# Performance work log

Measured on AMD Instinct MI355X. Metric: run time of the kernel, lower is better.

## Reference

```python
import jax, jax.numpy as jnp
import numpy as np
from jax import lax

HEADS = 4
SR = 4
LN_EPS = 1e-5


def setup_inputs() -> dict:
    key = jax.random.key(0)
    ks = jax.random.split(key, 8)
    B, N, C = 8, 4096, 256
    w_scale = 0.05  # keep attention logits in a sane range
    return {
        "x": jax.random.normal(ks[0], (B, N, C), jnp.float32),
        "h": 64,
        "w": 64,
        "Wq": jax.random.normal(ks[1], (C, C), jnp.float32) * w_scale,
        "Wkv": jax.random.normal(ks[2], (C, 2 * C), jnp.float32) * w_scale,
        "sr_w": jax.random.normal(ks[3], (C, C, SR, SR), jnp.float32) * w_scale,
        "sr_b": jnp.zeros((C,), jnp.float32),
        "ln_g": jnp.ones((C,), jnp.float32),
        "ln_b": jnp.zeros((C,), jnp.float32),
        "Wo": jax.random.normal(ks[4], (C, C), jnp.float32) * w_scale,
        "bo": jnp.zeros((C,), jnp.float32),
    }


def _layernorm(x, g, b):
    mu = x.mean(-1, keepdims=True)
    var = ((x - mu) ** 2).mean(-1, keepdims=True)
    return (x - mu) * lax.rsqrt(var + LN_EPS) * g + b


def reference(x, h, w, Wq, Wkv, sr_w, sr_b, ln_g, ln_b, Wo, bo):
    B, N, C = x.shape
    hd = C // HEADS
    scale = hd ** -0.5
    # Q projection -> [B, H, N, hd]
    q = (x @ Wq).reshape(B, N, HEADS, hd).transpose(0, 2, 1, 3)
    # spatial reduction of K/V tokens: strided conv + LayerNorm
    x_kv = x.transpose(0, 2, 1).reshape(B, C, h, w)  # b (h w) c -> b c h w
    x_kv = lax.conv_general_dilated(
        x_kv, sr_w, window_strides=(SR, SR), padding="VALID",
        dimension_numbers=("NCHW", "OIHW", "NCHW"))
    x_kv = x_kv + sr_b[None, :, None, None]
    Nk = (h // SR) * (w // SR)
    x_kv = x_kv.reshape(B, C, Nk).transpose(0, 2, 1)  # b c h w -> b (h w) c
    x_kv = _layernorm(x_kv, ln_g, ln_b)
    # KV projection -> k, v each [B, H, Nk, hd]
    kv = (x_kv @ Wkv).reshape(B, Nk, 2, HEADS, hd)
    k = kv[:, :, 0].transpose(0, 2, 1, 3)
    v = kv[:, :, 1].transpose(0, 2, 1, 3)
    # attention: full [B, H, N, Nk] score matrix, softmax over kv axis
    att = jax.nn.softmax(jnp.einsum("bhxd,bhyd->bhxy", q, k) * scale, axis=-1)
    out = jnp.einsum("bhxy,bhyd->bhxd", att, v)
    out = out.transpose(0, 2, 1, 3).reshape(B, N, C)  # b h l d -> b l (h d)
    return out @ Wo + bo
```

## Files before the change

kernel.cpp:

```cpp
#include <hip/hip_runtime.h>

typedef __bf16 bf16;
typedef bf16 bf16x8 __attribute__((ext_vector_type(8)));
typedef bf16 bf16x4 __attribute__((ext_vector_type(4)));
typedef float f32x4 __attribute__((ext_vector_type(4)));

#define MFMA16(a, b, c) __builtin_amdgcn_mfma_f32_16x16x32_bf16(a, b, c, 0, 0, 0)
#define WAIT_LDS() __builtin_amdgcn_s_waitcnt(0xC07F)

__global__ void k_prep(const float* __restrict__ x, const float* __restrict__ Wq,
                       const float* __restrict__ Wkv, const float* __restrict__ Wo,
                       const float* __restrict__ srw,
                       bf16* __restrict__ x_bf, bf16* __restrict__ WqT,
                       bf16* __restrict__ WkvT, bf16* __restrict__ WoT,
                       bf16* __restrict__ srwT) {
  int bid = blockIdx.x, tid = threadIdx.x;
  if (bid < 8192) {
    int i = (bid * 256 + tid) * 4;
    float4 v = *(const float4*)(x + i);
    bf16x4 o;
    o[0] = (bf16)v.x; o[1] = (bf16)v.y; o[2] = (bf16)v.z; o[3] = (bf16)v.w;
    *(bf16x4*)(x_bf + i) = o;
  } else if (bid < 9216) {
    int id = (bid - 8192) * 256 + tid;
    if (id < 65536) {
      int c = id >> 8, r = id & 255;
      WqT[id] = (bf16)Wq[r * 256 + c];
    } else if (id < 196608) {
      int l = id - 65536;
      int c = l >> 8, r = l & 255;
      WkvT[l] = (bf16)Wkv[r * 512 + c];
    } else {
      int l = id - 196608;
      int c = l >> 8, r = l & 255;
      WoT[l] = (bf16)Wo[r * 256 + c];
    }
  } else {
    int id4 = ((bid - 9216) * 256 + tid) * 4;
    int o = id4 >> 12, rem = id4 & 4095;
    int i = rem >> 4, p = rem & 15;
    float4 v = *(const float4*)(srw + id4);
    srwT[(o << 12) + ((p + 0) << 8) + i] = (bf16)v.x;
    srwT[(o << 12) + ((p + 1) << 8) + i] = (bf16)v.y;
    srwT[(o << 12) + ((p + 2) << 8) + i] = (bf16)v.z;
    srwT[(o << 12) + ((p + 3) << 8) + i] = (bf16)v.w;
  }
}

template <int AMODE, int EMODE>
__global__ __launch_bounds__(256, 2) void k_gemm(
    const bf16* __restrict__ A, const bf16* __restrict__ Bt,
    void* __restrict__ Cout, const float* __restrict__ bias,
    int M, int N, int K) {
  constexpr int LDT = 72;
  __shared__ alignas(16) bf16 As[64 * LDT];
  __shared__ alignas(16) bf16 Bs[64 * LDT];
  int tid = threadIdx.x;
  int m0 = blockIdx.x * 64, n0 = blockIdx.y * 64;
  int kbeg = blockIdx.z * K;
  int wave = tid >> 6, lane = tid & 63;
  int quad = lane >> 4, l16 = lane & 15;

  f32x4 acc[4];
#pragma unroll
  for (int i = 0; i < 4; i++) acc[i] = (f32x4){0.f, 0.f, 0.f, 0.f};

  for (int k0 = kbeg; k0 < kbeg + K; k0 += 64) {
#pragma unroll
    for (int t = 0; t < 2; t++) {
      int c = tid + t * 256;
      int row = c >> 3, c8 = (c & 7) * 8;
      const bf16* asrc;
      if constexpr (AMODE == 0) {
        asrc = A + (size_t)(m0 + row) * K + k0 + c8;
      } else {
        int m = m0 + row;
        int b = m >> 8, tt = m & 255;
        int oh = tt >> 4, ow = tt & 15;
        int p = k0 >> 8;
        int kh = p >> 2, kw = p & 3;
        int tok = (oh * 4 + kh) * 64 + ow * 4 + kw;
        asrc = A + ((size_t)(b * 4096 + tok) << 8) + (k0 & 255) + c8;
      }
      *(bf16x8*)&As[row * LDT + c8] = *(const bf16x8*)asrc;
      *(bf16x8*)&Bs[row * LDT + c8] =
          *(const bf16x8*)(Bt + (size_t)(n0 + row) * ((AMODE == 1) ? 4096 : K) + k0 + c8);
    }
    __syncthreads();
#pragma unroll
    for (int kk = 0; kk < 64; kk += 32) {
      bf16x8 af = *(const bf16x8*)&As[(wave * 16 + l16) * LDT + kk + quad * 8];
#pragma unroll
      for (int nt = 0; nt < 4; nt++) {
        bf16x8 bfr = *(const bf16x8*)&Bs[(nt * 16 + l16) * LDT + kk + quad * 8];
        acc[nt] = MFMA16(af, bfr, acc[nt]);
      }
    }
    __syncthreads();
  }

  int rbase = m0 + wave * 16 + quad * 4;
#pragma unroll
  for (int nt = 0; nt < 4; nt++) {
    int col = n0 + nt * 16 + l16;
#pragma unroll
    for (int r = 0; r < 4; r++) {
      float v = acc[nt][r];
      int row = rbase + r;
      if constexpr (EMODE == 2) {
        int b = row >> 8, key = row & 255;
        int isv = col >> 8, c2 = col & 255;
        int hh = c2 >> 6, d = c2 & 63;
        int bh = b * 4 + hh;
        bf16* dst = (bf16*)Cout;
        if (isv == 0)
          dst[(((size_t)bh) * 256 + key) * 64 + d] = (bf16)v;
        else
          dst[32 * 256 * 64 + (((size_t)bh) * 64 + d) * 256 + key] = (bf16)v;
      } else if constexpr (EMODE == 3) {
        ((float*)Cout)[(size_t)row * N + col] = v + bias[col];
      } else {
        ((float*)Cout)[((size_t)blockIdx.z * M + row) * N + col] = v;
      }
    }
  }
}

__global__ void k_ln(const float* __restrict__ part, const float* __restrict__ srb,
                     const float* __restrict__ g, const float* __restrict__ bb,
                     bf16* __restrict__ out) {
  int row = blockIdx.x * 4 + (threadIdx.x >> 6);
  int lane = threadIdx.x & 63;
  size_t off = (size_t)row * 256 + lane * 4;
  float4 v = *(const float4*)&part[off];
#pragma unroll
  for (int z = 1; z < 8; z++) {
    float4 p = *(const float4*)&part[(size_t)z * 2048 * 256 + off];
    v.x += p.x; v.y += p.y; v.z += p.z; v.w += p.w;
  }
  int c = lane * 4;
  v.x += srb[c + 0]; v.y += srb[c + 1]; v.z += srb[c + 2]; v.w += srb[c + 3];
  float s = v.x + v.y + v.z + v.w;
#pragma unroll
  for (int i = 1; i < 64; i <<= 1) s += __shfl_xor(s, i, 64);
  float mu = s * (1.f / 256.f);
  float d0 = v.x - mu, d1 = v.y - mu, d2 = v.z - mu, d3 = v.w - mu;
  float q = d0 * d0 + d1 * d1 + d2 * d2 + d3 * d3;
#pragma unroll
  for (int i = 1; i < 64; i <<= 1) q += __shfl_xor(q, i, 64);
  float rs = rsqrtf(q * (1.f / 256.f) + 1e-5f);
  bf16x4 o;
  o[0] = (bf16)(d0 * rs * g[c + 0] + bb[c + 0]);
  o[1] = (bf16)(d1 * rs * g[c + 1] + bb[c + 1]);
  o[2] = (bf16)(d2 * rs * g[c + 2] + bb[c + 2]);
  o[3] = (bf16)(d3 * rs * g[c + 3] + bb[c + 3]);
  *(bf16x4*)&out[(size_t)row * 256 + c] = o;
}

__global__ __launch_bounds__(256, 2) void k_attn(
    const bf16* __restrict__ xbf,
    const bf16* __restrict__ WqT,
    const bf16* __restrict__ Kb,
    const bf16* __restrict__ Vt_g,
    bf16* __restrict__ O) {
  int qt = blockIdx.x, bh = blockIdx.y;
  int b = bh >> 2, h = bh & 3;
  int tid = threadIdx.x, wave = tid >> 6, lane = tid & 63;
  int quad = lane >> 4, l16 = lane & 15;

  __shared__ alignas(16) bf16 Ks[256 * 72];
  __shared__ alignas(16) bf16 Vt[64 * 264];
  __shared__ alignas(16) bf16 Qs[64 * 72];

  const bf16* Kbh = Kb + (size_t)bh * 256 * 64;
  const bf16* Vbh = Vt_g + (size_t)bh * 64 * 256;

#pragma unroll
  for (int t = 0; t < 8; t++) {
    int c = tid + t * 256;
    *(bf16x8*)&Ks[(c >> 3) * 72 + (c & 7) * 8] = *(const bf16x8*)&Kbh[c * 8];
    *(bf16x8*)&Vt[(c >> 5) * 264 + (c & 31) * 8] = *(const bf16x8*)&Vbh[c * 8];
  }

  const bf16* xrow  = xbf + ((size_t)(b * 4096 + qt * 64 + wave * 16 + l16) << 8) + quad * 8;
  const bf16* wqrow = WqT + ((size_t)(h * 64) << 8);
  f32x4 q[4];
#pragma unroll
  for (int i = 0; i < 4; i++) q[i] = (f32x4){0.f, 0.f, 0.f, 0.f};
#pragma unroll
  for (int k0 = 0; k0 < 256; k0 += 32) {
    bf16x8 ax = *(const bf16x8*)(xrow + k0);
#pragma unroll
    for (int nt = 0; nt < 4; nt++) {
      bf16x8 bw = *(const bf16x8*)&wqrow[((size_t)(nt * 16 + l16) << 8) + k0 + quad * 8];
      q[nt] = MFMA16(ax, bw, q[nt]);
    }
  }

#pragma unroll
  for (int nt = 0; nt < 4; nt++)
#pragma unroll
    for (int r = 0; r < 4; r++)
      Qs[(wave * 16 + quad * 4 + r) * 72 + nt * 16 + l16] = (bf16)q[nt][r];
  WAIT_LDS();
  bf16x8 aq0 = *(const bf16x8*)&Qs[(wave * 16 + l16) * 72 + 0 + quad * 8];
  bf16x8 aq1 = *(const bf16x8*)&Qs[(wave * 16 + l16) * 72 + 32 + quad * 8];
  __syncthreads();

  f32x4 s[16];
#pragma unroll
  for (int i = 0; i < 16; i++) s[i] = (f32x4){0.f, 0.f, 0.f, 0.f};
#pragma unroll
  for (int nt = 0; nt < 16; nt++) {
    bf16x8 b0 = *(const bf16x8*)&Ks[(nt * 16 + l16) * 72 + 0 + quad * 8];
    bf16x8 b1 = *(const bf16x8*)&Ks[(nt * 16 + l16) * 72 + 32 + quad * 8];
    s[nt] = MFMA16(aq0, b0, s[nt]);
    s[nt] = MFMA16(aq1, b1, s[nt]);
  }

  const float scale = 0.125f;
#pragma unroll
  for (int r = 0; r < 4; r++) {
    float m = -1e30f;
#pragma unroll
    for (int nt = 0; nt < 16; nt++) m = fmaxf(m, s[nt][r]);
#pragma unroll
    for (int i = 1; i < 16; i <<= 1) m = fmaxf(m, __shfl_xor(m, i, 64));
    float sum = 0.f;
#pragma unroll
    for (int nt = 0; nt < 16; nt++) {
      float e = __expf((s[nt][r] - m) * scale);
      s[nt][r] = e;
      sum += e;
    }
#pragma unroll
    for (int i = 1; i < 16; i <<= 1) sum += __shfl_xor(sum, i, 64);
    float inv = 1.f / sum;
#pragma unroll
    for (int nt = 0; nt < 16; nt++) s[nt][r] *= inv;
  }
  __syncthreads();

  bf16* Ps = Ks;
#pragma unroll
  for (int nt = 0; nt < 16; nt++)
#pragma unroll
    for (int r = 0; r < 4; r++)
      Ps[(wave * 16 + quad * 4 + r) * 264 + nt * 16 + l16] = (bf16)s[nt][r];
  WAIT_LDS();

  f32x4 o[4];
#pragma unroll
  for (int i = 0; i < 4; i++) o[i] = (f32x4){0.f, 0.f, 0.f, 0.f};
#pragma unroll
  for (int k0 = 0; k0 < 256; k0 += 32) {
    bf16x8 ap = *(const bf16x8*)&Ps[(wave * 16 + l16) * 264 + k0 + quad * 8];
#pragma unroll
    for (int nt = 0; nt < 4; nt++) {
      bf16x8 bv = *(const bf16x8*)&Vt[(nt * 16 + l16) * 264 + k0 + quad * 8];
      o[nt] = MFMA16(ap, bv, o[nt]);
    }
  }

  size_t orow = (size_t)b * 4096 + qt * 64 + wave * 16 + quad * 4;
#pragma unroll
  for (int nt = 0; nt < 4; nt++) {
    int col = h * 64 + nt * 16 + l16;
#pragma unroll
    for (int r = 0; r < 4; r++) O[(orow + r) * 256 + col] = (bf16)o[nt][r];
  }
}

extern "C" void kernel_launch(void* const* d_in, const int* in_sizes, int n_in,
                              void* d_out, int out_size, void* d_ws, size_t ws_size,
                              hipStream_t stream) {
  (void)in_sizes; (void)n_in; (void)out_size; (void)ws_size;
  const float* x   = (const float*)d_in[0];
  const float* Wq  = (const float*)d_in[3];
  const float* Wkv = (const float*)d_in[4];
  const float* srw = (const float*)d_in[5];
  const float* srb = (const float*)d_in[6];
  const float* lng = (const float*)d_in[7];
  const float* lnb = (const float*)d_in[8];
  const float* Wo  = (const float*)d_in[9];
  const float* bo  = (const float*)d_in[10];
  float* out = (float*)d_out;

  char* ws = (char*)d_ws;
  bf16*  x_bf  = (bf16*)(ws + 0);
  bf16*  AObuf = (bf16*)(ws + 16777216);
  float* convp = (float*)(ws + 33554432);
  bf16*  WqT   = (bf16*)(ws + 50331648);
  bf16*  WkvT  = (bf16*)(ws + 50462720);
  bf16*  WoT   = (bf16*)(ws + 50724864);
  bf16*  srwT  = (bf16*)(ws + 50855936);
  bf16*  xln   = (bf16*)(ws + 52953088);
  bf16*  kvbuf = (bf16*)(ws + 54001664);

  k_prep<<<10240, 256, 0, stream>>>(x, Wq, Wkv, Wo, srw, x_bf, WqT, WkvT, WoT, srwT);
  k_gemm<1, 4><<<dim3(32, 4, 8), 256, 0, stream>>>(x_bf, srwT, convp, nullptr, 2048, 256, 512);
  k_ln<<<512, 256, 0, stream>>>(convp, srb, lng, lnb, xln);
  k_gemm<0, 2><<<dim3(32, 8), 256, 0, stream>>>(xln, WkvT, kvbuf, nullptr, 2048, 512, 256);
  k_attn<<<dim3(64, 32), 256, 0, stream>>>(x_bf, WqT, kvbuf, kvbuf + (size_t)32 * 256 * 64, AObuf);
  k_gemm<0, 3><<<dim3(512, 4), 256, 0, stream>>>(AObuf, WoT, out, bo, 32768, 256, 256);
}
```

Baseline: 196.1 us.

## Make attention blocks persistent over four query tiles with register-resident Wq and prefetch

Each attention block now handles four consecutive 64-row query tiles, so K/V are loaded into LDS once per four tiles instead of once per tile. The Wq slice is kept in registers, and the next tile's x rows are loaded and projected to Q while the current tile's softmax and PV run, overlapping load latency with compute. Launch bounds drop to one block per SM-equivalent and the grid shrinks fourfold. The cost is much higher register use (32 bf16x8 for Wq plus prefetch buffers) and fewer blocks, which lowers occupancy and could leave CUs idle.

```diff
diff --git a/kernel.cpp b/kernel.cpp
--- a/kernel.cpp
+++ b/kernel.cpp
@@ -157,23 +157,25 @@
   *(bf16x4*)&out[(size_t)row * 256 + c] = o;
 }
 
-__global__ __launch_bounds__(256, 2) void k_attn(
+__global__ __launch_bounds__(256, 1) void k_attn(
     const bf16* __restrict__ xbf,
     const bf16* __restrict__ WqT,
     const bf16* __restrict__ Kb,
     const bf16* __restrict__ Vt_g,
     bf16* __restrict__ O) {
-  int qt = blockIdx.x, bh = blockIdx.y;
+  constexpr int ITERS = 4;
+  int qg = blockIdx.x, bh = blockIdx.y;
   int b = bh >> 2, h = bh & 3;
   int tid = threadIdx.x, wave = tid >> 6, lane = tid & 63;
   int quad = lane >> 4, l16 = lane & 15;
 
   __shared__ alignas(16) bf16 Ks[256 * 72];
   __shared__ alignas(16) bf16 Vt[64 * 264];
-  __shared__ alignas(16) bf16 Qs[64 * 72];
-
-  const bf16* Kbh = Kb + (size_t)bh * 256 * 64;
-  const bf16* Vbh = Vt_g + (size_t)bh * 64 * 256;
+  __shared__ alignas(16) bf16 Ps[64 * 264];
+
+  const bf16* Kbh   = Kb + (size_t)bh * 256 * 64;
+  const bf16* Vbh   = Vt_g + (size_t)bh * 64 * 256;
+  const bf16* wqrow = WqT + ((size_t)(h * 64) << 8);
 
 #pragma unroll
   for (int t = 0; t < 8; t++) {
@@ -182,92 +184,131 @@
     *(bf16x8*)&Vt[(c >> 5) * 264 + (c & 31) * 8] = *(const bf16x8*)&Vbh[c * 8];
   }
 
-  const bf16* xrow  = xbf + ((size_t)(b * 4096 + qt * 64 + wave * 16 + l16) << 8) + quad * 8;
-  const bf16* wqrow = WqT + ((size_t)(h * 64) << 8);
+  bf16x8 wqf[32];
+#pragma unroll
+  for (int k8 = 0; k8 < 8; k8++)
+#pragma unroll
+    for (int nt = 0; nt < 4; nt++)
+      wqf[k8 * 4 + nt] =
+          *(const bf16x8*)&wqrow[((size_t)(nt * 16 + l16) << 8) + k8 * 32 + quad * 8];
+
+  int qrow0 = b * 4096 + qg * (ITERS * 64) + wave * 16 + l16;
+  int pstripe = (wave * 16 + quad * 4) * 264;
+
   f32x4 q[4];
 #pragma unroll
   for (int i = 0; i < 4; i++) q[i] = (f32x4){0.f, 0.f, 0.f, 0.f};
-#pragma unroll
-  for (int k0 = 0; k0 < 256; k0 += 32) {
-    bf16x8 ax = *(const bf16x8*)(xrow + k0);
+  {
+    const bf16* xr = xbf + ((size_t)qrow0 << 8) + quad * 8;
+#pragma unroll
+    for (int k8 = 0; k8 < 8; k8++) {
+      bf16x8 ax = *(const bf16x8*)(xr + k8 * 32);
+#pragma unroll
+      for (int nt = 0; nt < 4; nt++) q[nt] = MFMA16(ax, wqf[k8 * 4 + nt], q[nt]);
+    }
+  }
+#pragma unroll
+  for (int nt = 0; nt < 4; nt++)
+#pragma unroll
+    for (int r = 0; r < 4; r++)
+      Ps[pstripe + r * 264 + nt * 16 + l16] = (bf16)q[nt][r];
+  WAIT_LDS();
+  bf16x8 aq0 = *(const bf16x8*)&Ps[(wave * 16 + l16) * 264 + 0 + quad * 8];
+  bf16x8 aq1 = *(const bf16x8*)&Ps[(wave * 16 + l16) * 264 + 32 + quad * 8];
+  __syncthreads();
+
+  for (int it = 0; it < ITERS; ++it) {
+    bool more = (it + 1 < ITERS);
+
+    f32x4 s[16];
+#pragma unroll
+    for (int i = 0; i < 16; i++) s[i] = (f32x4){0.f, 0.f, 0.f, 0.f};
+#pragma unroll
+    for (int nt = 0; nt < 16; nt++) {
+      bf16x8 b0 = *(const bf16x8*)&Ks[(nt * 16 + l16) * 72 + 0 + quad * 8];
+      bf16x8 b1 = *(const bf16x8*)&Ks[(nt * 16 + l16) * 72 + 32 + quad * 8];
+      s[nt] = MFMA16(aq0, b0, s[nt]);
+      s[nt] = MFMA16(aq1, b1, s[nt]);
+    }
+
+    bf16x8 xn[8];
+    if (more) {
+      const bf16* xr = xbf + ((size_t)(qrow0 + (it + 1) * 64) << 8) + quad * 8;
+#pragma unroll
+      for (int k8 = 0; k8 < 8; k8++) xn[k8] = *(const bf16x8*)(xr + k8 * 32);
+    }
+
+    const float scale = 0.125f;
+#pragma unroll
+    for (int r = 0; r < 4; r++) {
+      float m = -1e30f;
+#pragma unroll
+      for (int nt = 0; nt < 16; nt++) m = fmaxf(m, s[nt][r]);
+#pragma unroll
+      for (int i = 1; i < 16; i <<= 1) m = fmaxf(m, __shfl_xor(m, i, 64));
+      float sum = 0.f;
+#pragma unroll
+      for (int nt = 0; nt < 16; nt++) {
+        float e = __expf((s[nt][r] - m) * scale);
+        s[nt][r] = e;
+        sum += e;
+      }
+#pragma unroll
+      for (int i = 1; i < 16; i <<= 1) sum += __shfl_xor(sum, i, 64);
+      float inv = 1.f / sum;
+#pragma unroll
+      for (int nt = 0; nt < 16; nt++) s[nt][r] *= inv;
+    }
+
+    f32x4 qn[4];
+#pragma unroll
+    for (int i = 0; i < 4; i++) qn[i] = (f32x4){0.f, 0.f, 0.f, 0.f};
+    if (more) {
+#pragma unroll
+      for (int k8 = 0; k8 < 8; k8++)
+#pragma unroll
+        for (int nt = 0; nt < 4; nt++)
+          qn[nt] = MFMA16(xn[k8], wqf[k8 * 4 + nt], qn[nt]);
+    }
+
+#pragma unroll
+    for (int nt = 0; nt < 16; nt++)
+#pragma unroll
+      for (int r = 0; r < 4; r++)
+        Ps[pstripe + r * 264 + nt * 16 + l16] = (bf16)s[nt][r];
+    WAIT_LDS();
+
+    f32x4 o[4];
+#pragma unroll
+    for (int i = 0; i < 4; i++) o[i] = (f32x4){0.f, 0.f, 0.f, 0.f};
+#pragma unroll
+    for (int k0 = 0; k0 < 256; k0 += 32) {
+      bf16x8 ap = *(const bf16x8*)&Ps[(wave * 16 + l16) * 264 + k0 + quad * 8];
+#pragma unroll
+      for (int nt = 0; nt < 4; nt++) {
+        bf16x8 bv = *(const bf16x8*)&Vt[(nt * 16 + l16) * 264 + k0 + quad * 8];
+        o[nt] = MFMA16(ap, bv, o[nt]);
+      }
+    }
+
+    size_t orow = (size_t)(qrow0 - l16) + it * 64 + quad * 4;
 #pragma unroll
     for (int nt = 0; nt < 4; nt++) {
-      bf16x8 bw = *(const bf16x8*)&wqrow[((size_t)(nt * 16 + l16) << 8) + k0 + quad * 8];
-      q[nt] = MFMA16(ax, bw, q[nt]);
-    }
-  }
-
-#pragma unroll
-  for (int nt = 0; nt < 4; nt++)
-#pragma unroll
-    for (int r = 0; r < 4; r++)
-      Qs[(wave * 16 + quad * 4 + r) * 72 + nt * 16 + l16] = (bf16)q[nt][r];
-  WAIT_LDS();
-  bf16x8 aq0 = *(const bf16x8*)&Qs[(wave * 16 + l16) * 72 + 0 + quad * 8];
-  bf16x8 aq1 = *(const bf16x8*)&Qs[(wave * 16 + l16) * 72 + 32 + quad * 8];
-  __syncthreads();
-
-  f32x4 s[16];
-#pragma unroll
-  for (int i = 0; i < 16; i++) s[i] = (f32x4){0.f, 0.f, 0.f, 0.f};
-#pragma unroll
-  for (int nt = 0; nt < 16; nt++) {
-    bf16x8 b0 = *(const bf16x8*)&Ks[(nt * 16 + l16) * 72 + 0 + quad * 8];
-    bf16x8 b1 = *(const bf16x8*)&Ks[(nt * 16 + l16) * 72 + 32 + quad * 8];
-    s[nt] = MFMA16(aq0, b0, s[nt]);
-    s[nt] = MFMA16(aq1, b1, s[nt]);
-  }
-
-  const float scale = 0.125f;
-#pragma unroll
-  for (int r = 0; r < 4; r++) {
-    float m = -1e30f;
-#pragma unroll
-    for (int nt = 0; nt < 16; nt++) m = fmaxf(m, s[nt][r]);
-#pragma unroll
-    for (int i = 1; i < 16; i <<= 1) m = fmaxf(m, __shfl_xor(m, i, 64));
-    float sum = 0.f;
-#pragma unroll
-    for (int nt = 0; nt < 16; nt++) {
-      float e = __expf((s[nt][r] - m) * scale);
-      s[nt][r] = e;
-      sum += e;
-    }
-#pragma unroll
-    for (int i = 1; i < 16; i <<= 1) sum += __shfl_xor(sum, i, 64);
-    float inv = 1.f / sum;
-#pragma unroll
-    for (int nt = 0; nt < 16; nt++) s[nt][r] *= inv;
-  }
-  __syncthreads();
-
-  bf16* Ps = Ks;
-#pragma unroll
-  for (int nt = 0; nt < 16; nt++)
-#pragma unroll
-    for (int r = 0; r < 4; r++)
-      Ps[(wave * 16 + quad * 4 + r) * 264 + nt * 16 + l16] = (bf16)s[nt][r];
-  WAIT_LDS();
-
-  f32x4 o[4];
-#pragma unroll
-  for (int i = 0; i < 4; i++) o[i] = (f32x4){0.f, 0.f, 0.f, 0.f};
-#pragma unroll
-  for (int k0 = 0; k0 < 256; k0 += 32) {
-    bf16x8 ap = *(const bf16x8*)&Ps[(wave * 16 + l16) * 264 + k0 + quad * 8];
-#pragma unroll
-    for (int nt = 0; nt < 4; nt++) {
-      bf16x8 bv = *(const bf16x8*)&Vt[(nt * 16 + l16) * 264 + k0 + quad * 8];
-      o[nt] = MFMA16(ap, bv, o[nt]);
-    }
-  }
-
-  size_t orow = (size_t)b * 4096 + qt * 64 + wave * 16 + quad * 4;
-#pragma unroll
-  for (int nt = 0; nt < 4; nt++) {
-    int col = h * 64 + nt * 16 + l16;
-#pragma unroll
-    for (int r = 0; r < 4; r++) O[(orow + r) * 256 + col] = (bf16)o[nt][r];
+      int col = h * 64 + nt * 16 + l16;
+#pragma unroll
+      for (int r = 0; r < 4; r++) O[(orow + r) * 256 + col] = (bf16)o[nt][r];
+    }
+
+    if (more) {
+#pragma unroll
+      for (int nt = 0; nt < 4; nt++)
+#pragma unroll
+        for (int r = 0; r < 4; r++)
+          Ps[pstripe + r * 264 + nt * 16 + l16] = (bf16)qn[nt][r];
+      WAIT_LDS();
+      aq0 = *(const bf16x8*)&Ps[(wave * 16 + l16) * 264 + 0 + quad * 8];
+      aq1 = *(const bf16x8*)&Ps[(wave * 16 + l16) * 264 + 32 + quad * 8];
+    }
   }
 }
 
@@ -301,6 +342,6 @@
   k_gemm<1, 4><<<dim3(32, 4, 8), 256, 0, stream>>>(x_bf, srwT, convp, nullptr, 2048, 256, 512);
   k_ln<<<512, 256, 0, stream>>>(convp, srb, lng, lnb, xln);
   k_gemm<0, 2><<<dim3(32, 8), 256, 0, stream>>>(xln, WkvT, kvbuf, nullptr, 2048, 512, 256);
-  k_attn<<<dim3(64, 32), 256, 0, stream>>>(x_bf, WqT, kvbuf, kvbuf + (size_t)32 * 256 * 64, AObuf);
+  k_attn<<<dim3(16, 32), 256, 0, stream>>>(x_bf, WqT, kvbuf, kvbuf + (size_t)32 * 256 * 64, AObuf);
   k_gemm<0, 3><<<dim3(512, 4), 256, 0, stream>>>(AObuf, WoT, out, bo, 32768, 256, 256);
 }
```

After: 200.1 us. 2.1% more time.

## Fuse x bf16 conversion into conv and attention loads; enlarge output GEMM tile

Applied to the files above, without the earlier changes.

Removes the separate pass that converted x to bf16. The conv and attention kernels now read fp32 x directly and convert it in registers, which saves a 32 MB read plus a 16 MB write and one large prep launch. The output projection GEMM gets its own kernel with a 128-row tile, two accumulator sets per wave and launch bounds of 4, to improve B-tile reuse. In exchange, the attention kernel reads twice as many bytes of x per Q tile, and the conv kernel does the same per A tile.

```diff
diff --git a/kernel.cpp b/kernel.cpp
--- a/kernel.cpp
+++ b/kernel.cpp
@@ -8,21 +8,20 @@
 #define MFMA16(a, b, c) __builtin_amdgcn_mfma_f32_16x16x32_bf16(a, b, c, 0, 0, 0)
 #define WAIT_LDS() __builtin_amdgcn_s_waitcnt(0xC07F)
 
-__global__ void k_prep(const float* __restrict__ x, const float* __restrict__ Wq,
-                       const float* __restrict__ Wkv, const float* __restrict__ Wo,
-                       const float* __restrict__ srw,
-                       bf16* __restrict__ x_bf, bf16* __restrict__ WqT,
-                       bf16* __restrict__ WkvT, bf16* __restrict__ WoT,
-                       bf16* __restrict__ srwT) {
+static __device__ __forceinline__ bf16x8 cvt8(float4 a, float4 b) {
+  bf16x8 r;
+  r[0] = (bf16)a.x; r[1] = (bf16)a.y; r[2] = (bf16)a.z; r[3] = (bf16)a.w;
+  r[4] = (bf16)b.x; r[5] = (bf16)b.y; r[6] = (bf16)b.z; r[7] = (bf16)b.w;
+  return r;
+}
+
+__global__ void k_prep(const float* __restrict__ Wq, const float* __restrict__ Wkv,
+                       const float* __restrict__ Wo, const float* __restrict__ srw,
+                       bf16* __restrict__ WqT, bf16* __restrict__ WkvT,
+                       bf16* __restrict__ WoT, bf16* __restrict__ srwT) {
   int bid = blockIdx.x, tid = threadIdx.x;
-  if (bid < 8192) {
-    int i = (bid * 256 + tid) * 4;
-    float4 v = *(const float4*)(x + i);
-    bf16x4 o;
-    o[0] = (bf16)v.x; o[1] = (bf16)v.y; o[2] = (bf16)v.z; o[3] = (bf16)v.w;
-    *(bf16x4*)(x_bf + i) = o;
-  } else if (bid < 9216) {
-    int id = (bid - 8192) * 256 + tid;
+  if (bid < 1024) {
+    int id = bid * 256 + tid;
     if (id < 65536) {
       int c = id >> 8, r = id & 255;
       WqT[id] = (bf16)Wq[r * 256 + c];
@@ -36,7 +35,7 @@
       WoT[l] = (bf16)Wo[r * 256 + c];
     }
   } else {
-    int id4 = ((bid - 9216) * 256 + tid) * 4;
+    int id4 = ((bid - 1024) * 256 + tid) * 4;
     int o = id4 >> 12, rem = id4 & 4095;
     int i = rem >> 4, p = rem & 15;
     float4 v = *(const float4*)(srw + id4);
@@ -47,11 +46,9 @@
   }
 }
 
-template <int AMODE, int EMODE>
-__global__ __launch_bounds__(256, 2) void k_gemm(
-    const bf16* __restrict__ A, const bf16* __restrict__ Bt,
-    void* __restrict__ Cout, const float* __restrict__ bias,
-    int M, int N, int K) {
+__global__ __launch_bounds__(256, 2) void k_conv(
+    const float* __restrict__ x, const bf16* __restrict__ Bt,
+    float* __restrict__ Cout, int M, int N, int K) {
   constexpr int LDT = 72;
   __shared__ alignas(16) bf16 As[64 * LDT];
   __shared__ alignas(16) bf16 Bs[64 * LDT];
@@ -70,21 +67,18 @@
     for (int t = 0; t < 2; t++) {
       int c = tid + t * 256;
       int row = c >> 3, c8 = (c & 7) * 8;
-      const bf16* asrc;
-      if constexpr (AMODE == 0) {
-        asrc = A + (size_t)(m0 + row) * K + k0 + c8;
-      } else {
-        int m = m0 + row;
-        int b = m >> 8, tt = m & 255;
-        int oh = tt >> 4, ow = tt & 15;
-        int p = k0 >> 8;
-        int kh = p >> 2, kw = p & 3;
-        int tok = (oh * 4 + kh) * 64 + ow * 4 + kw;
-        asrc = A + ((size_t)(b * 4096 + tok) << 8) + (k0 & 255) + c8;
-      }
-      *(bf16x8*)&As[row * LDT + c8] = *(const bf16x8*)asrc;
+      int m = m0 + row;
+      int b = m >> 8, tt = m & 255;
+      int oh = tt >> 4, ow = tt & 15;
+      int p = k0 >> 8;
+      int kh = p >> 2, kw = p & 3;
+      int tok = (oh * 4 + kh) * 64 + ow * 4 + kw;
+      const float* asrc = x + ((size_t)(b * 4096 + tok) << 8) + (k0 & 255) + c8;
+      float4 a0 = *(const float4*)asrc;
+      float4 a1 = *(const float4*)(asrc + 4);
+      *(bf16x8*)&As[row * LDT + c8] = cvt8(a0, a1);
       *(bf16x8*)&Bs[row * LDT + c8] =
-          *(const bf16x8*)(Bt + (size_t)(n0 + row) * ((AMODE == 1) ? 4096 : K) + k0 + c8);
+          *(const bf16x8*)(Bt + (size_t)(n0 + row) * 4096 + k0 + c8);
     }
     __syncthreads();
 #pragma unroll
@@ -104,24 +98,123 @@
   for (int nt = 0; nt < 4; nt++) {
     int col = n0 + nt * 16 + l16;
 #pragma unroll
+    for (int r = 0; r < 4; r++)
+      Cout[((size_t)blockIdx.z * M + rbase + r) * N + col] = acc[nt][r];
+  }
+}
+
+__global__ __launch_bounds__(256, 2) void k_kv(
+    const bf16* __restrict__ A, const bf16* __restrict__ Bt,
+    bf16* __restrict__ Cout, int M, int N, int K) {
+  constexpr int LDT = 72;
+  __shared__ alignas(16) bf16 As[64 * LDT];
+  __shared__ alignas(16) bf16 Bs[64 * LDT];
+  int tid = threadIdx.x;
+  int m0 = blockIdx.x * 64, n0 = blockIdx.y * 64;
+  int wave = tid >> 6, lane = tid & 63;
+  int quad = lane >> 4, l16 = lane & 15;
+
+  f32x4 acc[4];
+#pragma unroll
+  for (int i = 0; i < 4; i++) acc[i] = (f32x4){0.f, 0.f, 0.f, 0.f};
+
+  for (int k0 = 0; k0 < K; k0 += 64) {
+#pragma unroll
+    for (int t = 0; t < 2; t++) {
+      int c = tid + t * 256;
+      int row = c >> 3, c8 = (c & 7) * 8;
+      *(bf16x8*)&As[row * LDT + c8] = *(const bf16x8*)(A + (size_t)(m0 + row) * K + k0 + c8);
+      *(bf16x8*)&Bs[row * LDT + c8] = *(const bf16x8*)(Bt + (size_t)(n0 + row) * K + k0 + c8);
+    }
+    __syncthreads();
+#pragma unroll
+    for (int kk = 0; kk < 64; kk += 32) {
+      bf16x8 af = *(const bf16x8*)&As[(wave * 16 + l16) * LDT + kk + quad * 8];
+#pragma unroll
+      for (int nt = 0; nt < 4; nt++) {
+        bf16x8 bfr = *(const bf16x8*)&Bs[(nt * 16 + l16) * LDT + kk + quad * 8];
+        acc[nt] = MFMA16(af, bfr, acc[nt]);
+      }
+    }
+    __syncthreads();
+  }
+
+  int rbase = m0 + wave * 16 + quad * 4;
+#pragma unroll
+  for (int nt = 0; nt < 4; nt++) {
+    int col = n0 + nt * 16 + l16;
+#pragma unroll
     for (int r = 0; r < 4; r++) {
       float v = acc[nt][r];
       int row = rbase + r;
-      if constexpr (EMODE == 2) {
-        int b = row >> 8, key = row & 255;
-        int isv = col >> 8, c2 = col & 255;
-        int hh = c2 >> 6, d = c2 & 63;
-        int bh = b * 4 + hh;
-        bf16* dst = (bf16*)Cout;
-        if (isv == 0)
-          dst[(((size_t)bh) * 256 + key) * 64 + d] = (bf16)v;
-        else
-          dst[32 * 256 * 64 + (((size_t)bh) * 64 + d) * 256 + key] = (bf16)v;
-      } else if constexpr (EMODE == 3) {
-        ((float*)Cout)[(size_t)row * N + col] = v + bias[col];
-      } else {
-        ((float*)Cout)[((size_t)blockIdx.z * M + row) * N + col] = v;
+      int b = row >> 8, key = row & 255;
+      int isv = col >> 8, c2 = col & 255;
+      int hh = c2 >> 6, d = c2 & 63;
+      int bh = b * 4 + hh;
+      if (isv == 0)
+        Cout[(((size_t)bh) * 256 + key) * 64 + d] = (bf16)v;
+      else
+        Cout[32 * 256 * 64 + (((size_t)bh) * 64 + d) * 256 + key] = (bf16)v;
+    }
+  }
+}
+
+__global__ __launch_bounds__(256, 4) void k_out(
+    const bf16* __restrict__ A, const bf16* __restrict__ Bt,
+    float* __restrict__ C, const float* __restrict__ bias,
+    int M, int N, int K) {
+  constexpr int LDT = 72;
+  __shared__ alignas(16) bf16 As[128 * LDT];
+  __shared__ alignas(16) bf16 Bs[64 * LDT];
+  int tid = threadIdx.x;
+  int m0 = blockIdx.x * 128, n0 = blockIdx.y * 64;
+  int wave = tid >> 6, lane = tid & 63;
+  int quad = lane >> 4, l16 = lane & 15;
+
+  f32x4 acc0[4], acc1[4];
+#pragma unroll
+  for (int i = 0; i < 4; i++) {
+    acc0[i] = (f32x4){0.f, 0.f, 0.f, 0.f};
+    acc1[i] = (f32x4){0.f, 0.f, 0.f, 0.f};
+  }
+
+  for (int k0 = 0; k0 < K; k0 += 64) {
+#pragma unroll
+    for (int t = 0; t < 4; t++) {
+      int c = tid + t * 256;
+      int row = c >> 3, c8 = (c & 7) * 8;
+      *(bf16x8*)&As[row * LDT + c8] = *(const bf16x8*)(A + (size_t)(m0 + row) * K + k0 + c8);
+    }
+#pragma unroll
+    for (int t = 0; t < 2; t++) {
+      int c = tid + t * 256;
+      int row = c >> 3, c8 = (c & 7) * 8;
+      *(bf16x8*)&Bs[row * LDT + c8] = *(const bf16x8*)(Bt + (size_t)(n0 + row) * K + k0 + c8);
+    }
+    __syncthreads();
+#pragma unroll
+    for (int kk = 0; kk < 64; kk += 32) {
+      bf16x8 af0 = *(const bf16x8*)&As[(wave * 32 + l16) * LDT + kk + quad * 8];
+      bf16x8 af1 = *(const bf16x8*)&As[(wave * 32 + 16 + l16) * LDT + kk + quad * 8];
+#pragma unroll
+      for (int nt = 0; nt < 4; nt++) {
+        bf16x8 bfr = *(const bf16x8*)&Bs[(nt * 16 + l16) * LDT + kk + quad * 8];
+        acc0[nt] = MFMA16(af0, bfr, acc0[nt]);
+        acc1[nt] = MFMA16(af1, bfr, acc1[nt]);
       }
+    }
+    __syncthreads();
+  }
+
+  int rb0 = m0 + wave * 32 + quad * 4;
+#pragma unroll
+  for (int nt = 0; nt < 4; nt++) {
+    int col = n0 + nt * 16 + l16;
+    float bv = bias[col];
+#pragma unroll
+    for (int r = 0; r < 4; r++) {
+      C[(size_t)(rb0 + r) * N + col] = acc0[nt][r] + bv;
+      C[(size_t)(rb0 + 16 + r) * N + col] = acc1[nt][r] + bv;
     }
   }
 }
@@ -158,7 +251,7 @@
 }
 
 __global__ __launch_bounds__(256, 2) void k_attn(
-    const bf16* __restrict__ xbf,
+    const float* __restrict__ x,
     const bf16* __restrict__ WqT,
     const bf16* __restrict__ Kb,
     const bf16* __restrict__ Vt_g,
@@ -182,14 +275,16 @@
     *(bf16x8*)&Vt[(c >> 5) * 264 + (c & 31) * 8] = *(const bf16x8*)&Vbh[c * 8];
   }
 
-  const bf16* xrow  = xbf + ((size_t)(b * 4096 + qt * 64 + wave * 16 + l16) << 8) + quad * 8;
+  const float* xrow = x + ((size_t)(b * 4096 + qt * 64 + wave * 16 + l16) << 8) + quad * 8;
   const bf16* wqrow = WqT + ((size_t)(h * 64) << 8);
   f32x4 q[4];
 #pragma unroll
   for (int i = 0; i < 4; i++) q[i] = (f32x4){0.f, 0.f, 0.f, 0.f};
 #pragma unroll
   for (int k0 = 0; k0 < 256; k0 += 32) {
-    bf16x8 ax = *(const bf16x8*)(xrow + k0);
+    float4 xa = *(const float4*)(xrow + k0);
+    float4 xb = *(const float4*)(xrow + k0 + 4);
+    bf16x8 ax = cvt8(xa, xb);
 #pragma unroll
     for (int nt = 0; nt < 4; nt++) {
       bf16x8 bw = *(const bf16x8*)&wqrow[((size_t)(nt * 16 + l16) << 8) + k0 + quad * 8];
@@ -287,20 +382,19 @@
   float* out = (float*)d_out;
 
   char* ws = (char*)d_ws;
-  bf16*  x_bf  = (bf16*)(ws + 0);
-  bf16*  AObuf = (bf16*)(ws + 16777216);
-  float* convp = (float*)(ws + 33554432);
-  bf16*  WqT   = (bf16*)(ws + 50331648);
-  bf16*  WkvT  = (bf16*)(ws + 50462720);
-  bf16*  WoT   = (bf16*)(ws + 50724864);
-  bf16*  srwT  = (bf16*)(ws + 50855936);
-  bf16*  xln   = (bf16*)(ws + 52953088);
-  bf16*  kvbuf = (bf16*)(ws + 54001664);
-
-  k_prep<<<10240, 256, 0, stream>>>(x, Wq, Wkv, Wo, srw, x_bf, WqT, WkvT, WoT, srwT);
-  k_gemm<1, 4><<<dim3(32, 4, 8), 256, 0, stream>>>(x_bf, srwT, convp, nullptr, 2048, 256, 512);
+  bf16*  AObuf = (bf16*)(ws + 0);
+  float* convp = (float*)(ws + 16777216);
+  bf16*  WqT   = (bf16*)(ws + 33554432);
+  bf16*  WkvT  = (bf16*)(ws + 33685504);
+  bf16*  WoT   = (bf16*)(ws + 33947648);
+  bf16*  srwT  = (bf16*)(ws + 34078720);
+  bf16*  xln   = (bf16*)(ws + 36175872);
+  bf16*  kvbuf = (bf16*)(ws + 37224448);
+
+  k_prep<<<2048, 256, 0, stream>>>(Wq, Wkv, Wo, srw, WqT, WkvT, WoT, srwT);
+  k_conv<<<dim3(32, 4, 8), 256, 0, stream>>>(x, srwT, convp, 2048, 256, 512);
   k_ln<<<512, 256, 0, stream>>>(convp, srb, lng, lnb, xln);
-  k_gemm<0, 2><<<dim3(32, 8), 256, 0, stream>>>(xln, WkvT, kvbuf, nullptr, 2048, 512, 256);
-  k_attn<<<dim3(64, 32), 256, 0, stream>>>(x_bf, WqT, kvbuf, kvbuf + (size_t)32 * 256 * 64, AObuf);
-  k_gemm<0, 3><<<dim3(512, 4), 256, 0, stream>>>(AObuf, WoT, out, bo, 32768, 256, 256);
-}
+  k_kv<<<dim3(32, 8), 256, 0, stream>>>(xln, WkvT, kvbuf, 2048, 512, 256);
+  k_attn<<<dim3(64, 32), 256, 0, stream>>>(x, WqT, kvbuf, kvbuf + (size_t)32 * 256 * 64, AObuf);
+  k_out<<<dim3(256, 4), 256, 0, stream>>>(AObuf, WoT, out, bo, 32768, 256, 256);
+}
```

After: 206.4 us. 1.05x slower.
